# Optimization experiments

Hardware: AMD Instinct MI355X
Metric: run time of the kernel (lower is better)

The kernel has to match this reference:

```python
import jax, jax.numpy as jnp
import numpy as np

N_COUNTIES = 3144
P = 2
N_MOB = 6
N_COV = 10
T = 156
NNZ = 31440


def setup_inputs() -> dict:
    key = jax.random.key(0)
    ks = jax.random.split(key, 13)
    C = jax.random.uniform(ks[0], (T, N_COUNTIES), dtype=jnp.float32)
    D = jax.random.uniform(ks[1], (T, N_COUNTIES), dtype=jnp.float32)
    M = jax.random.uniform(ks[2], (N_MOB, T, N_COUNTIES), dtype=jnp.float32)
    cov = jax.random.normal(ks[3], (N_COV, N_COUNTIES), dtype=jnp.float32)
    B_nonzero = jax.random.normal(ks[4], (NNZ,), dtype=jnp.float32)
    A_nonzero = jax.random.normal(ks[5], (NNZ,), dtype=jnp.float32)
    H_nonzero = jax.random.normal(ks[6], (NNZ,), dtype=jnp.float32)
    mu = jax.random.normal(ks[7], (N_MOB, P), dtype=jnp.float32)
    nu = jax.random.normal(ks[8], (N_MOB, P), dtype=jnp.float32)
    upsilon = jax.random.normal(ks[9], (N_COV,), dtype=jnp.float32)
    zeta = jax.random.normal(ks[10], (N_COV,), dtype=jnp.float32)
    rows = jax.random.randint(ks[11], (NNZ,), 0, N_COUNTIES)
    cols = jax.random.randint(ks[12], (NNZ,), 0, N_COUNTIES)
    return dict(C=C, D=D, M=M, cov=cov, B_nonzero=B_nonzero, A_nonzero=A_nonzero,
                H_nonzero=H_nonzero, mu=mu, nu=nu, upsilon=upsilon, zeta=zeta,
                rows=rows, cols=cols)


def reference(C, D, M, cov, B_nonzero, A_nonzero, H_nonzero, mu, nu, upsilon, zeta, rows, cols):
    n = C.shape[1]
    p = mu.shape[1]
    Tp = C.shape[0] - p  # number of predicted steps (t = p .. T-1)

    # Dense scatter-built weight matrices (duplicates summed, matching
    # torch.sparse .to_dense()). The torch code reuses the SAME nonzero
    # vector for every lag tau, so B[tau] == B for all tau.
    B = jnp.zeros((n, n), C.dtype).at[rows, cols].add(B_nonzero)
    A = jnp.zeros((n, n), C.dtype).at[rows, cols].add(A_nonzero)
    H = jnp.zeros((n, n), C.dtype).at[rows, cols].add(H_nonzero)

    # Lagged windows: Cl[tau, i] = C[i + tau] == C[t - p + tau] for t = p + i.
    Cl = jnp.stack([C[tau:tau + Tp] for tau in range(p)], 0)  # [p, Tp, n]
    Dl = jnp.stack([D[tau:tau + Tp] for tau in range(p)], 0)  # [p, Tp, n]
    Ml = jnp.stack([M[:, tau:tau + Tp, :] for tau in range(p)], 1)  # [n_mob, p, Tp, n]

    # Since B[tau] are identical across lags, sum over p folds into one GEMM.
    c2c = jnp.einsum('ptn,nm->tm', Cl, B)  # [Tp, n]
    c2d = jnp.einsum('ptn,nm->tm', Cl, H)
    d2d = jnp.einsum('ptn,nm->tm', Dl, A)

    mob_c = jnp.einsum('kptn,kp->tn', Ml, mu)
    mob_d = jnp.einsum('kptn,kp->tn', Ml, nu)

    C_hat = c2c + mob_c + upsilon @ cov  # [Tp, n] (+ broadcast [n])
    D_hat = c2d + d2d + mob_d + zeta @ cov
    return C_hat, D_hat
```

## Files before the change

### kernel.cpp

```cpp
#include <hip/hip_runtime.h>


#define BS      256
#define ECAP    64
#define SPILLC  4096
#define SCAN_TH 1024

__global__ void prep(const int* __restrict__ rows, const int* __restrict__ cols,
                     const float* __restrict__ Bnz, const float* __restrict__ Anz,
                     const float* __restrict__ Hnz,
                     const float* __restrict__ C, const float* __restrict__ D,
                     float* __restrict__ Ct, float* __restrict__ Dt,
                     float4* __restrict__ edges, int* __restrict__ cnt,
                     int* __restrict__ spill_cnt, int* __restrict__ spill,
                     int T, int NC, int NNZ, int fillBlocks, int cT64, int tT64) {
    if ((int)blockIdx.x < fillBlocks) {
        int k = blockIdx.x * BS + threadIdx.x;
        if (k < NNZ) {
            int c = cols[k];
            int j = atomicAdd(&cnt[c], 1);
            if (j < ECAP)
                edges[(size_t)c * ECAP + j] =
                    make_float4(__int_as_float(rows[k]), Bnz[k], Anz[k], Hnz[k]);
            else {
                int sp = atomicAdd(spill_cnt, 1);
                if (sp < SPILLC) spill[sp] = k;
            }
        }
        return;
    }
    __shared__ float tile[64][65];
    int bid = blockIdx.x - fillBlocks;
    int tTiles = cT64 * tT64;
    int z = bid / tTiles;
    int r = bid - z * tTiles;
    int ct = r / tT64, tt = r - ct * tT64;
    const float* src = z ? D : C;
    float* dst = z ? Dt : Ct;
    int lx = threadIdx.x & 63, ly = threadIdx.x >> 6;
    int c0 = ct * 64, t0 = tt * 64;
    for (int rr = ly; rr < 64; rr += 4) {
        int t = t0 + rr, c = c0 + lx;
        if (t < T && c < NC) tile[rr][lx] = src[(size_t)t * NC + c];
    }
    __syncthreads();
    for (int rr = ly; rr < 64; rr += 4) {
        int c = c0 + rr, t = t0 + lx;
        if (c < NC && t < T) dst[(size_t)c * T + t] = tile[lx][rr];
    }
}

__global__ void sparse_wave(const float* __restrict__ Ct, const float* __restrict__ Dt,
                            const int* __restrict__ cnt, const float4* __restrict__ edges,
                            float* __restrict__ wsS0, float* __restrict__ wsS1,
                            int T, int TPn, int nChunks, int nWaves) {
    int gtid = blockIdx.x * blockDim.x + threadIdx.x;
    int wid = gtid >> 6, lane = threadIdx.x & 63;
    if (wid >= nWaves) return;
    int c = wid / nChunks;
    int chunk = wid - c * nChunks;
    int i = chunk * 64 + lane;
    bool valid = i < TPn;
    int isafe = valid ? i : 0;
    float a0 = 0.f, a1 = 0.f;
    int n = cnt[c]; if (n > ECAP) n = ECAP;
    const float4* eb = edges + (size_t)c * ECAP;
    for (int j = 0; j < n; ++j) {
        float4 E = eb[j];
        int g = __float_as_int(E.x);
        const float* cr = Ct + (size_t)g * T;
        const float* dr = Dt + (size_t)g * T;
        float cs = cr[isafe] + cr[isafe + 1];
        float ds = dr[isafe] + dr[isafe + 1];
        a0 += cs * E.y;
        a1 += cs * E.w + ds * E.z;
    }
    if (valid) {
        wsS0[(size_t)c * TPn + i] = a0;
        wsS1[(size_t)c * TPn + i] = a1;
    }
}

#define FTI 32
#define FTC 32
__global__ void final_fuse(const float* __restrict__ wsS0, const float* __restrict__ wsS1,
                           const float* __restrict__ M,
                           const float* __restrict__ cov,
                           const float* __restrict__ mu,
                           const float* __restrict__ nu,
                           const float* __restrict__ ups, const float* __restrict__ zet,
                           const float* __restrict__ Ct, const float* __restrict__ Dt,
                           const int* __restrict__ rows, const int* __restrict__ cols,
                           const float* __restrict__ Bnz, const float* __restrict__ Anz,
                           const float* __restrict__ Hnz,
                           const int* __restrict__ spill_cnt, const int* __restrict__ spill,
                           float* __restrict__ out0, float* __restrict__ out1,
                           int T, int NC, int TPn, int cTiles) {
    __shared__ float s0[FTI][FTC + 1], s1[FTI][FTC + 1];
    int bi = blockIdx.x / cTiles;
    int bc = blockIdx.x - bi * cTiles;
    int i0 = bi * FTI, c0 = bc * FTC;
    int tid = threadIdx.x;

    {
        int li = tid & 31;
        int lc0 = tid >> 5;
        int i = i0 + li;
        for (int cc = lc0; cc < FTC; cc += 8) {
            int c = c0 + cc;
            float v0 = 0.f, v1 = 0.f;
            if (c < NC && i < TPn) {
                v0 = wsS0[(size_t)c * TPn + i];
                v1 = wsS1[(size_t)c * TPn + i];
            }
            s0[li][cc] = v0;
            s1[li][cc] = v1;
        }
    }
    __syncthreads();

    int lc = tid & 31;
    int ri = tid >> 5;
    int c = c0 + lc;
    if (c < NC) {
        float cv0 = 0.f, cv1 = 0.f;
#pragma unroll
        for (int j = 0; j < 10; ++j) {
            float cv = cov[(size_t)j * NC + c];
            cv0 += cv * ups[j];
            cv1 += cv * zet[j];
        }
        int iiBeg = ri * 4;
        int iFirst = i0 + iiBeg;
        if (iFirst < TPn) {
            float m0r[6];
#pragma unroll
            for (int k = 0; k < 6; ++k)
                m0r[k] = M[((size_t)k * T + iFirst) * NC + c];
#pragma unroll
            for (int ii = 0; ii < 4; ++ii) {
                int i = iFirst + ii;
                if (i >= TPn) break;
                float a0 = s0[iiBeg + ii][lc] + cv0;
                float a1 = s1[iiBeg + ii][lc] + cv1;
#pragma unroll
                for (int k = 0; k < 6; ++k) {
                    float m1 = M[((size_t)k * T + i + 1) * NC + c];
                    a0 += m0r[k] * mu[k * 2] + m1 * mu[k * 2 + 1];
                    a1 += m0r[k] * nu[k * 2] + m1 * nu[k * 2 + 1];
                    m0r[k] = m1;
                }
                out0[(size_t)i * NC + c] = a0;
                out1[(size_t)i * NC + c] = a1;
            }
        }
    }

    int nsp = *spill_cnt;
    if (nsp > 0) {
        __syncthreads();
        if (nsp > SPILLC) nsp = SPILLC;
        int cmax = NC - c0; if (cmax > FTC) cmax = FTC;
        if (tid < FTI) {
            int io = i0 + tid;
            if (io < TPn) {
                for (int s = 0; s < nsp; ++s) {
                    int k = spill[s];
                    int cc = cols[k];
                    if (cc >= c0 && cc < c0 + cmax) {
                        int g = rows[k];
                        float cs = Ct[(size_t)g * T + io] + Ct[(size_t)g * T + io + 1];
                        float ds = Dt[(size_t)g * T + io] + Dt[(size_t)g * T + io + 1];
                        atomicAdd(&out0[(size_t)io * NC + cc], cs * Bnz[k]);
                        atomicAdd(&out1[(size_t)io * NC + cc], cs * Hnz[k] + ds * Anz[k]);
                    }
                }
            }
        }
    }
}

__global__ void csr_hist(const int* __restrict__ cols, int* __restrict__ counts, int NNZ) {
    int k = blockIdx.x * blockDim.x + threadIdx.x;
    if (k < NNZ) atomicAdd(&counts[cols[k]], 1);
}
__global__ __launch_bounds__(SCAN_TH)
void csr_scan(const int* __restrict__ counts, int* __restrict__ offsets,
              int* __restrict__ cursor, int NC) {
    __shared__ int ssum[SCAN_TH];
    int t = threadIdx.x;
    int chunk = (NC + SCAN_TH - 1) / SCAN_TH;
    int beg = t * chunk, end = min(beg + chunk, NC);
    int local = 0;
    for (int j = beg; j < end; ++j) local += counts[j];
    ssum[t] = local;
    __syncthreads();
    for (int off = 1; off < SCAN_TH; off <<= 1) {
        int v = (t >= off) ? ssum[t - off] : 0;
        __syncthreads();
        ssum[t] += v;
        __syncthreads();
    }
    int run = ssum[t] - local;
    for (int j = beg; j < end; ++j) {
        offsets[j] = run;
        cursor[j]  = run;
        run += counts[j];
    }
    if (t == SCAN_TH - 1) offsets[NC] = ssum[SCAN_TH - 1];
}
__global__ void csr_fill(const int* __restrict__ rows, const int* __restrict__ cols,
                         const float* __restrict__ Bnz, const float* __restrict__ Anz,
                         const float* __restrict__ Hnz,
                         int* __restrict__ cursor, float4* __restrict__ edges, int NNZ) {
    int k = blockIdx.x * blockDim.x + threadIdx.x;
    if (k >= NNZ) return;
    int s = cols[k];
    int pos = atomicAdd(&cursor[s], 1);
    edges[pos] = make_float4(__int_as_float(rows[k]), Bnz[k], Anz[k], Hnz[k]);
}
__global__ void fused_generic(const float* __restrict__ C, const float* __restrict__ D,
                              const float* __restrict__ M, const float* __restrict__ cov,
                              const float* __restrict__ mu, const float* __restrict__ nu,
                              const float* __restrict__ ups, const float* __restrict__ zet,
                              const int* __restrict__ offsets, const float4* __restrict__ edges,
                              float* __restrict__ out0, float* __restrict__ out1,
                              int T, int NC, int NMOB, int NCOV, int P, int TPn) {
    int idx = blockIdx.x * blockDim.x + threadIdx.x;
    if (idx >= TPn * NC) return;
    int i = idx / NC;
    int c = idx - i * NC;
    float acc0 = 0.f, acc1 = 0.f;
    for (int k = 0; k < NMOB; ++k)
        for (int tau = 0; tau < P; ++tau) {
            float m = M[((size_t)k * T + i + tau) * NC + c];
            acc0 += m * mu[k * P + tau];
            acc1 += m * nu[k * P + tau];
        }
    for (int j = 0; j < NCOV; ++j) {
        float cv = cov[(size_t)j * NC + c];
        acc0 += cv * ups[j];
        acc1 += cv * zet[j];
    }
    int e0 = offsets[c], e1 = offsets[c + 1];
    for (int e = e0; e < e1; ++e) {
        float4 E = edges[e];
        int g = __float_as_int(E.x);
        float cs = 0.f, ds = 0.f;
        for (int tau = 0; tau < P; ++tau) {
            cs += C[(size_t)(i + tau) * NC + g];
            ds += D[(size_t)(i + tau) * NC + g];
        }
        acc0 += cs * E.y;
        acc1 += cs * E.w + ds * E.z;
    }
    out0[idx] = acc0;
    out1[idx] = acc1;
}

extern "C" void kernel_launch(void* const* d_in, const int* in_sizes, int n_in,
                              void* d_out, int out_size, void* d_ws, size_t ws_size,
                              hipStream_t stream) {
    const float* C    = (const float*)d_in[0];
    const float* D    = (const float*)d_in[1];
    const float* M    = (const float*)d_in[2];
    const float* cov  = (const float*)d_in[3];
    const float* Bnz  = (const float*)d_in[4];
    const float* Anz  = (const float*)d_in[5];
    const float* Hnz  = (const float*)d_in[6];
    const float* mu   = (const float*)d_in[7];
    const float* nu   = (const float*)d_in[8];
    const float* ups  = (const float*)d_in[9];
    const float* zet  = (const float*)d_in[10];
    const int*  rows  = (const int*)d_in[11];
    const int*  cols  = (const int*)d_in[12];

    int NCOV = in_sizes[9];
    int NC   = in_sizes[3] / NCOV;
    int T    = in_sizes[0] / NC;
    int NMOB = in_sizes[2] / in_sizes[0];
    int P    = in_sizes[7] / NMOB;
    int NNZ  = in_sizes[11];
    int TPn  = T - P;

    float* out0 = (float*)d_out;
    float* out1 = out0 + (size_t)TPn * NC;

    float4* edges  = (float4*)d_ws;
    int*    cnt    = (int*)(edges + (size_t)NC * ECAP);
    int*    spillc = cnt + NC;
    int*    spill  = spillc + 1;
    float*  Ct     = (float*)(spill + SPILLC);
    float*  Dt     = Ct + (size_t)NC * T;
    float*  wsS0   = Dt + (size_t)NC * T;
    float*  wsS1   = wsS0 + (size_t)NC * TPn;
    size_t  need   = (size_t)((char*)(wsS1 + (size_t)NC * TPn) - (char*)d_ws);

    if (P == 2 && NMOB == 6 && NCOV == 10 && ws_size >= need) {
        hipMemsetAsync(cnt, 0, (size_t)(NC + 1) * sizeof(int), stream);

        int fillBlocks = (NNZ + BS - 1) / BS;
        int cT64 = (NC + 63) / 64, tT64 = (T + 63) / 64;
        prep<<<fillBlocks + 2 * cT64 * tT64, BS, 0, stream>>>(
            rows, cols, Bnz, Anz, Hnz, C, D, Ct, Dt,
            edges, cnt, spillc, spill, T, NC, NNZ, fillBlocks, cT64, tT64);

        int nChunks = (TPn + 63) / 64;
        int nWaves  = NC * nChunks;
        sparse_wave<<<(nWaves * 64 + BS - 1) / BS, BS, 0, stream>>>(
            Ct, Dt, cnt, edges, wsS0, wsS1, T, TPn, nChunks, nWaves);

        int iTiles = (TPn + FTI - 1) / FTI;
        int cTiles = (NC + FTC - 1) / FTC;
        final_fuse<<<iTiles * cTiles, BS, 0, stream>>>(
            wsS0, wsS1, M, cov, mu, nu, ups, zet, Ct, Dt,
            rows, cols, Bnz, Anz, Hnz, spillc, spill,
            out0, out1, T, NC, TPn, cTiles);
    } else {
        float4* fedges   = (float4*)d_ws;
        int*    foffsets = (int*)(fedges + NNZ);
        int*    fcounts  = foffsets + (NC + 1);
        int*    fcursor  = fcounts + NC;
        hipMemsetAsync(fcounts, 0, (size_t)NC * sizeof(int), stream);
        csr_hist<<<(NNZ + BS - 1) / BS, BS, 0, stream>>>(cols, fcounts, NNZ);
        csr_scan<<<1, SCAN_TH, 0, stream>>>(fcounts, foffsets, fcursor, NC);
        csr_fill<<<(NNZ + BS - 1) / BS, BS, 0, stream>>>(
            rows, cols, Bnz, Anz, Hnz, fcursor, fedges, NNZ);
        int n = TPn * NC;
        fused_generic<<<(n + BS - 1) / BS, BS, 0, stream>>>(
            C, D, M, cov, mu, nu, ups, zet, foffsets, fedges,
            out0, out1, T, NC, NMOB, NCOV, P, TPn);
    }
}
```

Baseline: 123.3 us.

## Precompute lag-summed C/D into interleaved float2 layout for the gather

The transpose stage now adds the two lags of C and D in shared memory and writes an interleaved float2 array of lag sums per county. The sparse gather then does one 8-byte load per edge instead of four scalar loads from two arrays, and the intermediate results are stored as float2 as well. The aim is fewer gather transactions and less memory traffic in the hot sparse kernel. In exchange the transpose tile is larger, with extra shared-memory rows for the lag overlap, and the workspace pointer is realigned to 16 bytes.

After: 121.1 us. Within noise of the previous version (-1.9%).

```diff
diff --git a/kernel.cpp b/kernel.cpp
--- a/kernel.cpp
+++ b/kernel.cpp
@@ -10,10 +10,10 @@
                      const float* __restrict__ Bnz, const float* __restrict__ Anz,
                      const float* __restrict__ Hnz,
                      const float* __restrict__ C, const float* __restrict__ D,
-                     float* __restrict__ Ct, float* __restrict__ Dt,
+                     float2* __restrict__ CsDs,
                      float4* __restrict__ edges, int* __restrict__ cnt,
                      int* __restrict__ spill_cnt, int* __restrict__ spill,
-                     int T, int NC, int NNZ, int fillBlocks, int cT64, int tT64) {
+                     int T, int NC, int NNZ, int TPn, int fillBlocks, int tT64) {
     if ((int)blockIdx.x < fillBlocks) {
         int k = blockIdx.x * BS + threadIdx.x;
         if (k < NNZ) {
@@ -29,67 +29,63 @@
         }
         return;
     }
-    __shared__ float tile[64][65];
+    __shared__ float tc[65][65], td[65][65];
     int bid = blockIdx.x - fillBlocks;
-    int tTiles = cT64 * tT64;
-    int z = bid / tTiles;
-    int r = bid - z * tTiles;
-    int ct = r / tT64, tt = r - ct * tT64;
-    const float* src = z ? D : C;
-    float* dst = z ? Dt : Ct;
+    int ct = bid / tT64, tt = bid - ct * tT64;
     int lx = threadIdx.x & 63, ly = threadIdx.x >> 6;
     int c0 = ct * 64, t0 = tt * 64;
-    for (int rr = ly; rr < 64; rr += 4) {
+    for (int rr = ly; rr < 65; rr += 4) {
         int t = t0 + rr, c = c0 + lx;
-        if (t < T && c < NC) tile[rr][lx] = src[(size_t)t * NC + c];
+        if (t < T && c < NC) {
+            tc[rr][lx] = C[(size_t)t * NC + c];
+            td[rr][lx] = D[(size_t)t * NC + c];
+        }
     }
     __syncthreads();
     for (int rr = ly; rr < 64; rr += 4) {
         int c = c0 + rr, t = t0 + lx;
-        if (c < NC && t < T) dst[(size_t)c * T + t] = tile[lx][rr];
-    }
-}
-
-__global__ void sparse_wave(const float* __restrict__ Ct, const float* __restrict__ Dt,
+        if (c < NC && t < TPn)
+            CsDs[(size_t)c * TPn + t] =
+                make_float2(tc[lx][rr] + tc[lx + 1][rr],
+                            td[lx][rr] + td[lx + 1][rr]);
+    }
+}
+
+__global__ void sparse_wave(const float2* __restrict__ CsDs,
                             const int* __restrict__ cnt, const float4* __restrict__ edges,
-                            float* __restrict__ wsS0, float* __restrict__ wsS1,
-                            int T, int TPn, int nChunks, int nWaves) {
+                            float2* __restrict__ wsS,
+                            int TPn, int nChunks, int nWaves) {
     int gtid = blockIdx.x * blockDim.x + threadIdx.x;
     int wid = gtid >> 6, lane = threadIdx.x & 63;
     if (wid >= nWaves) return;
     int c = wid / nChunks;
     int chunk = wid - c * nChunks;
+    int cu = __builtin_amdgcn_readfirstlane(c);
     int i = chunk * 64 + lane;
     bool valid = i < TPn;
-    int isafe = valid ? i : 0;
+    int isafe = valid ? i : (TPn - 1);
     float a0 = 0.f, a1 = 0.f;
-    int n = cnt[c]; if (n > ECAP) n = ECAP;
-    const float4* eb = edges + (size_t)c * ECAP;
+    int n = cnt[cu]; if (n > ECAP) n = ECAP;
+    const float4* eb = edges + (size_t)cu * ECAP;
     for (int j = 0; j < n; ++j) {
         float4 E = eb[j];
         int g = __float_as_int(E.x);
-        const float* cr = Ct + (size_t)g * T;
-        const float* dr = Dt + (size_t)g * T;
-        float cs = cr[isafe] + cr[isafe + 1];
-        float ds = dr[isafe] + dr[isafe + 1];
-        a0 += cs * E.y;
-        a1 += cs * E.w + ds * E.z;
-    }
-    if (valid) {
-        wsS0[(size_t)c * TPn + i] = a0;
-        wsS1[(size_t)c * TPn + i] = a1;
-    }
+        float2 v = CsDs[(size_t)g * TPn + isafe];
+        a0 += v.x * E.y;
+        a1 += v.x * E.w + v.y * E.z;
+    }
+    if (valid) wsS[(size_t)c * TPn + i] = make_float2(a0, a1);
 }
 
 #define FTI 32
 #define FTC 32
-__global__ void final_fuse(const float* __restrict__ wsS0, const float* __restrict__ wsS1,
+__global__ void final_fuse(const float2* __restrict__ wsS,
                            const float* __restrict__ M,
                            const float* __restrict__ cov,
                            const float* __restrict__ mu,
                            const float* __restrict__ nu,
                            const float* __restrict__ ups, const float* __restrict__ zet,
-                           const float* __restrict__ Ct, const float* __restrict__ Dt,
+                           const float2* __restrict__ CsDs,
                            const int* __restrict__ rows, const int* __restrict__ cols,
                            const float* __restrict__ Bnz, const float* __restrict__ Anz,
                            const float* __restrict__ Hnz,
@@ -108,13 +104,10 @@
         int i = i0 + li;
         for (int cc = lc0; cc < FTC; cc += 8) {
             int c = c0 + cc;
-            float v0 = 0.f, v1 = 0.f;
-            if (c < NC && i < TPn) {
-                v0 = wsS0[(size_t)c * TPn + i];
-                v1 = wsS1[(size_t)c * TPn + i];
-            }
-            s0[li][cc] = v0;
-            s1[li][cc] = v1;
+            float2 v = make_float2(0.f, 0.f);
+            if (c < NC && i < TPn) v = wsS[(size_t)c * TPn + i];
+            s0[li][cc] = v.x;
+            s1[li][cc] = v.y;
         }
     }
     __syncthreads();
@@ -169,10 +162,9 @@
                     int cc = cols[k];
                     if (cc >= c0 && cc < c0 + cmax) {
                         int g = rows[k];
-                        float cs = Ct[(size_t)g * T + io] + Ct[(size_t)g * T + io + 1];
-                        float ds = Dt[(size_t)g * T + io] + Dt[(size_t)g * T + io + 1];
-                        atomicAdd(&out0[(size_t)io * NC + cc], cs * Bnz[k]);
-                        atomicAdd(&out1[(size_t)io * NC + cc], cs * Hnz[k] + ds * Anz[k]);
+                        float2 v = CsDs[(size_t)g * TPn + io];
+                        atomicAdd(&out0[(size_t)io * NC + cc], v.x * Bnz[k]);
+                        atomicAdd(&out1[(size_t)io * NC + cc], v.x * Hnz[k] + v.y * Anz[k]);
                     }
                 }
             }
@@ -290,30 +282,30 @@
     int*    cnt    = (int*)(edges + (size_t)NC * ECAP);
     int*    spillc = cnt + NC;
     int*    spill  = spillc + 1;
-    float*  Ct     = (float*)(spill + SPILLC);
-    float*  Dt     = Ct + (size_t)NC * T;
-    float*  wsS0   = Dt + (size_t)NC * T;
-    float*  wsS1   = wsS0 + (size_t)NC * TPn;
-    size_t  need   = (size_t)((char*)(wsS1 + (size_t)NC * TPn) - (char*)d_ws);
+    uintptr_t pa   = (uintptr_t)(spill + SPILLC);
+    pa             = (pa + 15) & ~(uintptr_t)15;
+    float2* CsDs   = (float2*)pa;
+    float2* wsS    = CsDs + (size_t)NC * TPn;
+    size_t  need   = (size_t)((char*)(wsS + (size_t)NC * TPn) - (char*)d_ws);
 
     if (P == 2 && NMOB == 6 && NCOV == 10 && ws_size >= need) {
         hipMemsetAsync(cnt, 0, (size_t)(NC + 1) * sizeof(int), stream);
 
         int fillBlocks = (NNZ + BS - 1) / BS;
         int cT64 = (NC + 63) / 64, tT64 = (T + 63) / 64;
-        prep<<<fillBlocks + 2 * cT64 * tT64, BS, 0, stream>>>(
-            rows, cols, Bnz, Anz, Hnz, C, D, Ct, Dt,
-            edges, cnt, spillc, spill, T, NC, NNZ, fillBlocks, cT64, tT64);
+        prep<<<fillBlocks + cT64 * tT64, BS, 0, stream>>>(
+            rows, cols, Bnz, Anz, Hnz, C, D, CsDs,
+            edges, cnt, spillc, spill, T, NC, NNZ, TPn, fillBlocks, tT64);
 
         int nChunks = (TPn + 63) / 64;
         int nWaves  = NC * nChunks;
         sparse_wave<<<(nWaves * 64 + BS - 1) / BS, BS, 0, stream>>>(
-            Ct, Dt, cnt, edges, wsS0, wsS1, T, TPn, nChunks, nWaves);
+            CsDs, cnt, edges, wsS, TPn, nChunks, nWaves);
 
         int iTiles = (TPn + FTI - 1) / FTI;
         int cTiles = (NC + FTC - 1) / FTC;
         final_fuse<<<iTiles * cTiles, BS, 0, stream>>>(
-            wsS0, wsS1, M, cov, mu, nu, ups, zet, Ct, Dt,
+            wsS, M, cov, mu, nu, ups, zet, CsDs,
             rows, cols, Bnz, Anz, Hnz, spillc, spill,
             out0, out1, T, NC, TPn, cTiles);
     } else {
```
